# Kernel tuning notes

Measured on AMD Instinct MI355X. Metric: run time of the kernel, lower is better.

Reference implementation:

```python
import jax, jax.numpy as jnp
import numpy as np
from jax.scipy.linalg import cho_solve

BLOCKSIZE = 128   # sharded_gptc.BLOCKSIZE
PERC_DAMP = 0.01


def _get_divisible_blocksize(dim: int, blocksize_top: int) -> int:
    b = blocksize_top
    while dim % b != 0:
        b -= 1
    return b


def setup_inputs() -> dict:
    key = jax.random.key(0)
    x = jax.random.normal(key, (4, 2048, 1024), dtype=jnp.float32)
    return {"x": x, "ca": 2}


def reference(x, ca):
    # --- reshape/transpose bookkeeping from GptqHinvCollector.__call__ ---
    ca_axes = (int(ca),)
    transpose = [a for a in range(x.ndim) if a not in ca_axes] + list(ca_axes)
    x = x.transpose(transpose)
    features = int(np.prod(x.shape[-len(ca_axes):]))
    x = x.reshape((-1, features))                      # (rows, F)
    blocksize = _get_divisible_blocksize(x.shape[0], BLOCKSIZE)
    xb = x.reshape((-1, blocksize, features))          # (nblocks, bs, F)

    # --- _init_hinv_for_calibration: damped diagonal initialization ---
    diag = jnp.mean(jnp.float32(xb) ** 2, (0, 1))      # (F,)
    damp = PERC_DAMP * jnp.mean(diag)
    hinv0 = jnp.diag(jnp.ones(features, jnp.float32) / damp)  # (damp*I)^-1

    # --- compute_hinv: blocked Woodbury / Cholesky recursion over row blocks ---
    # hinv_{k+1} = (hinv_k^{-1} + B^T B)^{-1}
    #            = hinv_k - hinv_k B^T (I + B hinv_k B^T)^{-1} B hinv_k
    eye_b = jnp.eye(blocksize, dtype=jnp.float32)

    def block_update(hinv, B):
        HB = hinv @ B.T                                # (F, bs)
        S = eye_b + B @ HB                             # (bs, bs), SPD
        L = jnp.linalg.cholesky(S)
        W = cho_solve((L, True), HB.T)                 # S^{-1} (B hinv): (bs, F)
        return hinv - HB @ W, None

    hinv, _ = jax.lax.scan(block_update, hinv0, xb)

    # act_order=False -> identity permutation
    perm = jnp.arange(features, dtype=jnp.int32)

    # CALIBRATE path after init: collected_hinv = hinv, num_calibrated_batches = 1
    num_calibrated_batches = jnp.int32(1)
    return hinv * num_calibrated_batches, perm
```

## Files before the change

kernel.cpp:

```cpp
#include <hip/hip_runtime.h>
#include <math.h>

#define F 1024
#define NROWS 8192
#define NELEM (NROWS * F)

typedef unsigned short ushort_t;
typedef short bf16x8 __attribute__((ext_vector_type(8)));
typedef float f32x4 __attribute__((ext_vector_type(4)));
typedef unsigned short ushort8 __attribute__((ext_vector_type(8)));

__device__ __forceinline__ ushort_t f2bf(float f) {
  unsigned u = __float_as_uint(f);
  unsigned r = (u + 0x7fffu + ((u >> 16) & 1u)) >> 16;
  return (ushort_t)r;
}
__device__ __forceinline__ float bf2f(ushort_t b) {
  return __uint_as_float(((unsigned)b) << 16);
}

typedef const __attribute__((address_space(1))) unsigned int* gas_ptr;
typedef __attribute__((address_space(3))) unsigned int* las_ptr;
__device__ __forceinline__ void gload16(const void* g, const void* l) {
  __builtin_amdgcn_global_load_lds((gas_ptr)(unsigned long long)g,
                                   (las_ptr)(unsigned int)(unsigned long long)l,
                                   16, 0, 0);
}

__global__ __launch_bounds__(256) void tconv_kernel(const float* __restrict__ x,
                                                    ushort_t* __restrict__ xthi,
                                                    ushort_t* __restrict__ xtlo,
                                                    float* __restrict__ partial) {
    __shared__ ushort_t th[64][68];
    __shared__ ushort_t tl[64][68];
    __shared__ float sdata[256];
    int c0 = blockIdx.x * 64;
    int r0 = blockIdx.y * 64;
    int tid = threadIdx.x;
    float ss = 0.f;
#pragma unroll
    for (int i = 0; i < 4; ++i) {
        int q = tid + 256 * i;
        int r = q >> 4;
        int cq = (q & 15) << 2;
        float4 vx = *(const float4*)&x[(size_t)(r0 + r) * 1024 + c0 + cq];
        float vv[4] = {vx.x, vx.y, vx.z, vx.w};
#pragma unroll
        for (int j = 0; j < 4; ++j) {
            ss = fmaf(vv[j], vv[j], ss);
            ushort_t h = f2bf(vv[j]);
            ushort_t l = f2bf(vv[j] - bf2f(h));
            th[r][cq + j] = h;
            tl[r][cq + j] = l;
        }
    }
    sdata[tid] = ss;
    __syncthreads();
    for (int off = 128; off > 0; off >>= 1) {
        if (tid < off) sdata[tid] += sdata[tid + off];
        __syncthreads();
    }
    if (tid == 0) partial[blockIdx.y * 16 + blockIdx.x] = sdata[0];
#pragma unroll
    for (int i = 0; i < 2; ++i) {
        int q = tid + 256 * i;
        int c = q >> 3;
        int rq = (q & 7) << 3;
        ushort8 oh, ol;
#pragma unroll
        for (int j = 0; j < 8; ++j) {
            oh[j] = th[rq + j][c];
            ol[j] = tl[rq + j][c];
        }
        *(ushort8*)&xthi[(size_t)(c0 + c) * 8192 + r0 + rq] = oh;
        *(ushort8*)&xtlo[(size_t)(c0 + c) * 8192 + r0 + rq] = ol;
    }
}

__global__ void finish_damp_kernel(const float* __restrict__ partial, float* __restrict__ scal) {
    __shared__ float sdata[256];
    int tid = threadIdx.x;
    float s = 0.f;
    for (int i = tid; i < 2048; i += 256) s += partial[i];
    sdata[tid] = s;
    __syncthreads();
    for (int off = 128; off > 0; off >>= 1) {
        if (tid < off) sdata[tid] += sdata[tid + off];
        __syncthreads();
    }
    if (tid == 0) {
        float mean = sdata[0] / (float)NELEM;
        scal[1] = 0.01f * mean;
    }
}

__device__ __forceinline__ void stage128(const ushort_t* __restrict__ gp, int row0, int kk,
                                         ushort_t* sbase, int w, int lane) {
#pragma unroll
    for (int half = 0; half < 2; ++half) {
        int s = half * 256 + (w << 6) + lane;
        int r = s >> 2, pos = s & 3;
        int kc = (pos ^ ((r >> 1) & 3)) << 3;
        gload16(gp + (size_t)(row0 + r) * 8192 + kk + kc,
                sbase + (size_t)((half << 8) + (w << 6)) * 8);
    }
}

template <int NZ>
__global__ __launch_bounds__(256, 2) void syrk_mfma_kernel(
    const ushort_t* __restrict__ XThi, const ushort_t* __restrict__ XTlo,
    float* __restrict__ P)
{
    constexpr int KCH = 8192 / NZ;
    constexpr int NKT = KCH / 32;
    __shared__ ushort_t smem[2][16384];
    int id = blockIdx.x;
    int z = id & (NZ - 1), t = id / NZ;
    int bi = 0;
    while ((bi + 1) * (bi + 2) / 2 <= t) ++bi;
    int bj = t - bi * (bi + 1) / 2;
    int arow0 = bi * 128, brow0 = bj * 128;
    int k0 = z * KCH;

    int tid = threadIdx.x, lane = tid & 63, w = tid >> 6;
    int wm = w >> 1, wn = w & 1;
    int lr = lane & 15, cg = lane >> 4;

    f32x4 zero4 = {0.f, 0.f, 0.f, 0.f};
    f32x4 acc[4][4];
#pragma unroll
    for (int a = 0; a < 4; ++a)
#pragma unroll
        for (int b = 0; b < 4; ++b) acc[a][b] = zero4;

#define SYRK_STAGE(BUF, KT)                                                        \
    {                                                                              \
        ushort_t* sb = smem[BUF];                                                  \
        int kk = k0 + ((KT) << 5);                                                 \
        stage128(XThi, arow0, kk, sb + 0, w, lane);                                \
        stage128(XTlo, arow0, kk, sb + 4096, w, lane);                             \
        stage128(XThi, brow0, kk, sb + 8192, w, lane);                             \
        stage128(XTlo, brow0, kk, sb + 12288, w, lane);                            \
    }

#define SYRK_COMPUTE(BUF)                                                          \
    {                                                                              \
        const ushort_t* sb = smem[BUF];                                            \
        bf16x8 ah[4], bh[4], al[4], bl[4];                                         \
        _Pragma("unroll")                                                          \
        for (int fx = 0; fx < 4; ++fx) {                                           \
            int xo = (cg ^ ((lr >> 1) & 3)) << 3;                                  \
            int ao = ((wm << 6) + (fx << 4) + lr) * 32 + xo;                       \
            int bo = ((wn << 6) + (fx << 4) + lr) * 32 + xo;                       \
            ah[fx] = *(const bf16x8*)&sb[0 + ao];                                  \
            al[fx] = *(const bf16x8*)&sb[4096 + ao];                               \
            bh[fx] = *(const bf16x8*)&sb[8192 + bo];                               \
            bl[fx] = *(const bf16x8*)&sb[12288 + bo];                              \
        }                                                                          \
        _Pragma("unroll")                                                          \
        for (int fm = 0; fm < 4; ++fm)                                             \
            _Pragma("unroll")                                                      \
            for (int fn = 0; fn < 4; ++fn) {                                       \
                acc[fm][fn] = __builtin_amdgcn_mfma_f32_16x16x32_bf16(             \
                    ah[fm], bh[fn], acc[fm][fn], 0, 0, 0);                         \
                acc[fm][fn] = __builtin_amdgcn_mfma_f32_16x16x32_bf16(             \
                    ah[fm], bl[fn], acc[fm][fn], 0, 0, 0);                         \
                acc[fm][fn] = __builtin_amdgcn_mfma_f32_16x16x32_bf16(             \
                    al[fm], bh[fn], acc[fm][fn], 0, 0, 0);                         \
            }                                                                      \
    }

    SYRK_STAGE(0, 0)
    for (int kt = 0; kt < NKT - 1; ++kt) {
        int buf = kt & 1;
        if (buf == 0) SYRK_STAGE(1, kt + 1) else SYRK_STAGE(0, kt + 1)
        asm volatile("s_waitcnt vmcnt(8)" ::: "memory");
        __builtin_amdgcn_s_barrier();
        __builtin_amdgcn_sched_barrier(0);
        if (buf == 0) SYRK_COMPUTE(0) else SYRK_COMPUTE(1)
        __builtin_amdgcn_sched_barrier(0);
        __builtin_amdgcn_s_barrier();
    }
    asm volatile("s_waitcnt vmcnt(0)" ::: "memory");
    __builtin_amdgcn_s_barrier();
    __builtin_amdgcn_sched_barrier(0);
    if (((NKT - 1) & 1) == 0) SYRK_COMPUTE(0) else SYRK_COMPUTE(1)

    float* Pt = P + ((size_t)(t * NZ + z) << 14);
#pragma unroll
    for (int fm = 0; fm < 4; ++fm)
#pragma unroll
        for (int fn = 0; fn < 4; ++fn)
#pragma unroll
            for (int rr = 0; rr < 4; ++rr) {
                int row = (wm << 6) + fm * 16 + cg * 4 + rr;
                int col = (wn << 6) + fn * 16 + lr;
                Pt[row * 128 + col] = acc[fm][fn][rr];
            }
}

template <int NZ>
__global__ void reduceH_kernel(const float* __restrict__ P,
                               ushort_t* __restrict__ Hhi, ushort_t* __restrict__ Hlo,
                               const float* __restrict__ scal) {
    int b = blockIdx.x;
    int tile = b >> 6;
    int li = ((b & 63) << 8) + threadIdx.x;
    int bi = 0;
    while ((bi + 1) * (bi + 2) / 2 <= tile) ++bi;
    int bj = tile - bi * (bi + 1) / 2;
    const float* Pt = P + (size_t)tile * NZ * 16384;
    float s = 0.f;
#pragma unroll
    for (int z = 0; z < NZ; ++z) s += Pt[((size_t)z << 14) + li];
    int r = li >> 7, c = li & 127;
    int gi = bi * 128 + r, gj = bj * 128 + c;
    if (gi == gj) s += scal[1];
    ushort_t h = f2bf(s), l = f2bf(s - bf2f(h));
    Hhi[gi * F + gj] = h;
    Hlo[gi * F + gj] = l;
    if (bi != bj) {
        Hhi[gj * F + gi] = h;
        Hlo[gj * F + gi] = l;
    }
}

__global__ void matvec_bf16_kernel(const ushort_t* __restrict__ Hhi, const float* __restrict__ v,
                                   float* __restrict__ y, int first) {
    __shared__ float sdata[256];
    int row = blockIdx.x, tid = threadIdx.x;
    float s = 0.f;
    if (first) {
        for (int j = tid; j < F; j += 256) s += bf2f(Hhi[row * F + j]);
    } else {
        for (int j = tid; j < F; j += 256) s = fmaf(bf2f(Hhi[row * F + j]), v[j], s);
    }
    sdata[tid] = s;
    __syncthreads();
    for (int off = 128; off > 0; off >>= 1) {
        if (tid < off) sdata[tid] += sdata[tid + off];
        __syncthreads();
    }
    if (tid == 0) y[row] = sdata[0];
}

__global__ void normalize_kernel(const float* __restrict__ y, float* __restrict__ v,
                                 float* __restrict__ scal) {
    __shared__ float sdata[256];
    __shared__ float lam;
    int tid = threadIdx.x;
    float s = 0.f;
    for (int i = tid; i < F; i += 256) {
        float t = y[i];
        s = fmaf(t, t, s);
    }
    sdata[tid] = s;
    __syncthreads();
    for (int off = 128; off > 0; off >>= 1) {
        if (tid < off) sdata[tid] += sdata[tid + off];
        __syncthreads();
    }
    if (tid == 0) {
        lam = sqrtf(sdata[0]);
        scal[2] = lam;
        scal[3] = 1.0f / (1.05f * lam);
    }
    __syncthreads();
    float il = 1.0f / lam;
    for (int i = tid; i < F; i += 256) v[i] = y[i] * il;
}

__global__ void initX1_kernel(const ushort_t* __restrict__ Hhi, const ushort_t* __restrict__ Hlo,
                              ushort_t* __restrict__ Xhi, ushort_t* __restrict__ Xlo,
                              const float* __restrict__ scal) {
    int idx0 = (blockIdx.x * 256 + threadIdx.x) * 4;
    float c = scal[3];
    float c2 = c * c;
#pragma unroll
    for (int k = 0; k < 4; ++k) {
        int idx = idx0 + k;
        float hv = bf2f(Hhi[idx]) + bf2f(Hlo[idx]);
        float val = -c2 * hv + (((idx >> 10) == (idx & 1023)) ? 2.f * c : 0.f);
        ushort_t h = f2bf(val);
        Xhi[idx] = h;
        Xlo[idx] = f2bf(val - bf2f(h));
    }
}

__device__ __forceinline__ void stage64(const ushort_t* __restrict__ gp, int row0, int kk,
                                        ushort_t* sbase, int tid) {
    int r = tid >> 2, pos = tid & 3;
    int kc = (pos ^ ((r >> 1) & 3)) << 3;
    gload16(gp + (size_t)(row0 + r) * 1024 + kk + kc, sbase + (size_t)(tid >> 6 << 9));
}

template <int TERMS, int MODE>
__global__ __launch_bounds__(256) void ns_gemm_kernel(
    const ushort_t* __restrict__ Ahi, const ushort_t* __restrict__ Alo,
    const ushort_t* __restrict__ Bhi, const ushort_t* __restrict__ Blo,
    const ushort_t* __restrict__ Xchi, const ushort_t* __restrict__ Xclo,
    ushort_t* __restrict__ Ohi, ushort_t* __restrict__ Olo,
    float* __restrict__ Of)
{
    constexpr int SLOT = (TERMS == 3) ? 8192 : 4096;
    __shared__ ushort_t smem[4 * SLOT];
    int tid = threadIdx.x, lane = tid & 63, w = tid >> 6;
    int wm = w >> 1, wn = w & 1;
    int row0 = blockIdx.y * 64, col0 = blockIdx.x * 64;
    int lr = lane & 15, cg = lane >> 4;

    f32x4 zero4 = {0.f, 0.f, 0.f, 0.f};
    f32x4 acc[2][2];
#pragma unroll
    for (int a = 0; a < 2; ++a)
#pragma unroll
        for (int b = 0; b < 2; ++b) acc[a][b] = zero4;

#define NS_STAGE(KT)                                                               \
    {                                                                              \
        ushort_t* sb = smem + (size_t)((KT) & 3) * SLOT;                           \
        int kk = (KT) << 5;                                                        \
        stage64(Ahi, row0, kk, sb + 0, tid);                                       \
        stage64(Bhi, col0, kk, sb + 2048, tid);                                    \
        if constexpr (TERMS == 3) {                                                \
            stage64(Alo, row0, kk, sb + 4096, tid);                                \
            stage64(Blo, col0, kk, sb + 6144, tid);                                \
        }                                                                          \
    }

#define NS_COMPUTE(KT)                                                             \
    {                                                                              \
        const ushort_t* sb = smem + (size_t)((KT) & 3) * SLOT;                     \
        bf16x8 ah[2], bh[2], al[2], bl[2];                                         \
        _Pragma("unroll")                                                          \
        for (int fx = 0; fx < 2; ++fx) {                                           \
            int xo = (cg ^ ((lr >> 1) & 3)) << 3;                                  \
            int ao = ((wm << 5) + (fx << 4) + lr) * 32 + xo;                       \
            int bo = ((wn << 5) + (fx << 4) + lr) * 32 + xo;                       \
            ah[fx] = *(const bf16x8*)&sb[0 + ao];                                  \
            bh[fx] = *(const bf16x8*)&sb[2048 + bo];                               \
            if constexpr (TERMS == 3) {                                            \
                al[fx] = *(const bf16x8*)&sb[4096 + ao];                           \
                bl[fx] = *(const bf16x8*)&sb[6144 + bo];                           \
            }                                                                      \
        }                                                                          \
        _Pragma("unroll")                                                          \
        for (int fm = 0; fm < 2; ++fm)                                             \
            _Pragma("unroll")                                                      \
            for (int fn = 0; fn < 2; ++fn) {                                       \
                acc[fm][fn] = __builtin_amdgcn_mfma_f32_16x16x32_bf16(             \
                    ah[fm], bh[fn], acc[fm][fn], 0, 0, 0);                         \
                if constexpr (TERMS == 3) {                                        \
                    acc[fm][fn] = __builtin_amdgcn_mfma_f32_16x16x32_bf16(         \
                        ah[fm], bl[fn], acc[fm][fn], 0, 0, 0);                     \
                    acc[fm][fn] = __builtin_amdgcn_mfma_f32_16x16x32_bf16(         \
                        al[fm], bh[fn], acc[fm][fn], 0, 0, 0);                     \
                }                                                                  \
            }                                                                      \
    }

    NS_STAGE(0)
    NS_STAGE(1)
    for (int kt = 0; kt < 30; ++kt) {
        NS_STAGE(kt + 2)
        if constexpr (TERMS == 3) { asm volatile("s_waitcnt vmcnt(8)" ::: "memory"); }
        else                      { asm volatile("s_waitcnt vmcnt(4)" ::: "memory"); }
        __builtin_amdgcn_s_barrier();
        __builtin_amdgcn_sched_barrier(0);
        NS_COMPUTE(kt)
        __builtin_amdgcn_sched_barrier(0);
    }
    if constexpr (TERMS == 3) { asm volatile("s_waitcnt vmcnt(4)" ::: "memory"); }
    else                      { asm volatile("s_waitcnt vmcnt(2)" ::: "memory"); }
    __builtin_amdgcn_s_barrier();
    __builtin_amdgcn_sched_barrier(0);
    NS_COMPUTE(30)
    asm volatile("s_waitcnt vmcnt(0)" ::: "memory");
    __builtin_amdgcn_s_barrier();
    __builtin_amdgcn_sched_barrier(0);
    NS_COMPUTE(31)

#pragma unroll
    for (int fm = 0; fm < 2; ++fm)
#pragma unroll
        for (int fn = 0; fn < 2; ++fn)
#pragma unroll
            for (int rr = 0; rr < 4; ++rr) {
                int r = row0 + (wm << 5) + fm * 16 + cg * 4 + rr;
                int c = col0 + (wn << 5) + fn * 16 + lr;
                size_t idx = (size_t)r * F + c;
                float val = acc[fm][fn][rr];
                if constexpr (MODE == 0) {
                    ushort_t h = f2bf(val);
                    Ohi[idx] = h;
                    Olo[idx] = f2bf(val - bf2f(h));
                } else {
                    float xc = bf2f(Xchi[idx]) + bf2f(Xclo[idx]);
                    val = 2.0f * xc - val;
                    if constexpr (MODE == 1) {
                        ushort_t h = f2bf(val);
                        Ohi[idx] = h;
                        Olo[idx] = f2bf(val - bf2f(h));
                    } else {
                        Of[idx] = val;
                    }
                }
            }
    if constexpr (MODE == 2) {
        if (blockIdx.x == 0 && blockIdx.y == 0) {
            int i0 = tid * 4;
#pragma unroll
            for (int k = 0; k < 4; ++k)
                Of[(size_t)F * F + i0 + k] = (float)(i0 + k);
        }
    }
}

__global__ void sumsq_partial_kernel(const float* __restrict__ x, float* __restrict__ partial) {
    __shared__ float sdata[256];
    int tid = threadIdx.x;
    int base = blockIdx.x * 4096;
    float s = 0.f;
    for (int i = tid; i < 4096; i += 256) {
        float v = x[base + i];
        s = fmaf(v, v, s);
    }
    sdata[tid] = s;
    __syncthreads();
    for (int off = 128; off > 0; off >>= 1) {
        if (tid < off) sdata[tid] += sdata[tid + off];
        __syncthreads();
    }
    if (tid == 0) partial[blockIdx.x] = sdata[0];
}

__global__ void init_v_kernel(float* __restrict__ v) {
    int i = blockIdx.x * 256 + threadIdx.x;
    if (i < F) v[i] = 1.0f;
}

__global__ void matvec_kernel(const float* __restrict__ H, const float* __restrict__ v,
                              float* __restrict__ y) {
    __shared__ float sdata[256];
    int row = blockIdx.x, tid = threadIdx.x;
    float s = 0.f;
    for (int j = tid; j < F; j += 256) s = fmaf(H[row * F + j], v[j], s);
    sdata[tid] = s;
    __syncthreads();
    for (int off = 128; off > 0; off >>= 1) {
        if (tid < off) sdata[tid] += sdata[tid + off];
        __syncthreads();
    }
    if (tid == 0) y[row] = sdata[0];
}

__global__ __launch_bounds__(256) void syrk_kernel(const float* __restrict__ X,
                                                   float* __restrict__ H,
                                                   const float* __restrict__ scal) {
    __shared__ float LA[16][64];
    __shared__ float LB[16][64];
    int tx = threadIdx.x, ty = threadIdx.y;
    int t = ty * 16 + tx;
    int i0 = blockIdx.y * 64, j0 = blockIdx.x * 64;
    int lk = t >> 4;
    int lc = (t & 15) << 2;
    float acc[4][4] = {};
    for (int k0 = 0; k0 < NROWS; k0 += 16) {
        int r = (k0 + lk) * F;
        float4 a4 = *(const float4*)&X[r + i0 + lc];
        float4 b4 = *(const float4*)&X[r + j0 + lc];
        __syncthreads();
        *(float4*)&LA[lk][lc] = a4;
        *(float4*)&LB[lk][lc] = b4;
        __syncthreads();
#pragma unroll
        for (int kk = 0; kk < 16; ++kk) {
            float4 a = *(const float4*)&LA[kk][ty << 2];
            float4 b = *(const float4*)&LB[kk][tx << 2];
            float av[4] = {a.x, a.y, a.z, a.w};
            float bv[4] = {b.x, b.y, b.z, b.w};
#pragma unroll
            for (int rr = 0; rr < 4; ++rr)
#pragma unroll
                for (int cc = 0; cc < 4; ++cc)
                    acc[rr][cc] = fmaf(av[rr], bv[cc], acc[rr][cc]);
        }
    }
    float damp = scal[1];
#pragma unroll
    for (int rr = 0; rr < 4; ++rr) {
        int i = i0 + (ty << 2) + rr;
#pragma unroll
        for (int cc = 0; cc < 4; ++cc) {
            int j = j0 + (tx << 2) + cc;
            float v = acc[rr][cc];
            if (i == j) v += damp;
            H[i * F + j] = v;
        }
    }
}

__global__ void init_X_kernel(float* __restrict__ A, const float* __restrict__ scal) {
    int idx = blockIdx.x * 256 + threadIdx.x;
    int i = idx >> 10, j = idx & (F - 1);
    A[idx] = (i == j) ? scal[3] : 0.0f;
}

__global__ __launch_bounds__(256) void gemm_nn_kernel(const float* __restrict__ A,
                                                      const float* __restrict__ Bm,
                                                      float* __restrict__ C,
                                                      const float* __restrict__ D,
                                                      int mode) {
    __shared__ float LA[16][64];
    __shared__ float LB[16][64];
    int tx = threadIdx.x, ty = threadIdx.y;
    int t = ty * 16 + tx;
    int i0 = blockIdx.y * 64, j0 = blockIdx.x * 64;
    int aii = t >> 2;
    int akq = (t & 3) << 2;
    int bkk = t >> 4;
    int bjq = (t & 15) << 2;
    float acc[4][4] = {};
    for (int k0 = 0; k0 < F; k0 += 16) {
        float4 a4 = *(const float4*)&A[(i0 + aii) * F + k0 + akq];
        float4 b4 = *(const float4*)&Bm[(k0 + bkk) * F + j0 + bjq];
        __syncthreads();
        LA[akq + 0][aii] = a4.x;
        LA[akq + 1][aii] = a4.y;
        LA[akq + 2][aii] = a4.z;
        LA[akq + 3][aii] = a4.w;
        *(float4*)&LB[bkk][bjq] = b4;
        __syncthreads();
#pragma unroll
        for (int kk = 0; kk < 16; ++kk) {
            float4 a = *(const float4*)&LA[kk][ty << 2];
            float4 b = *(const float4*)&LB[kk][tx << 2];
            float av[4] = {a.x, a.y, a.z, a.w};
            float bv[4] = {b.x, b.y, b.z, b.w};
#pragma unroll
            for (int rr = 0; rr < 4; ++rr)
#pragma unroll
                for (int cc = 0; cc < 4; ++cc)
                    acc[rr][cc] = fmaf(av[rr], bv[cc], acc[rr][cc]);
        }
    }
#pragma unroll
    for (int rr = 0; rr < 4; ++rr) {
        int i = i0 + (ty << 2) + rr;
#pragma unroll
        for (int cc = 0; cc < 4; ++cc) {
            int j = j0 + (tx << 2) + cc;
            float v = acc[rr][cc];
            if (mode == 1) v = 2.0f * D[i * F + j] - v;
            C[i * F + j] = v;
        }
    }
}

__global__ void finalize_kernel(const float* __restrict__ A, float* __restrict__ out) {
    int idx = blockIdx.x * 256 + threadIdx.x;
    if (idx < F * F) out[idx] = A[idx];
    else if (idx < F * F + F) out[idx] = (float)(idx - F * F);
}

extern "C" void kernel_launch(void* const* d_in, const int* in_sizes, int n_in,
                              void* d_out, int out_size, void* d_ws, size_t ws_size,
                              hipStream_t stream) {
    const float* x = (const float*)d_in[0];
    float* out = (float*)d_out;

    char* base = (char*)d_ws;
    size_t off = 0;
    auto alloc = [&](size_t bytes) -> char* {
        char* p = base + off;
        off += bytes;
        off = (off + 255) & ~(size_t)255;
        return p;
    };
    float*    scal = (float*)alloc(64 * 4);
    float*    part = (float*)alloc(2048 * 4);
    ushort_t* XThi = (ushort_t*)alloc((size_t)NELEM * 2);
    ushort_t* XTlo = (ushort_t*)alloc((size_t)NELEM * 2);
    ushort_t* Hhi  = (ushort_t*)alloc((size_t)F * F * 2);
    ushort_t* Hlo  = (ushort_t*)alloc((size_t)F * F * 2);
    ushort_t* X0hi = (ushort_t*)alloc((size_t)F * F * 2);
    ushort_t* X0lo = (ushort_t*)alloc((size_t)F * F * 2);
    ushort_t* X1hi = (ushort_t*)alloc((size_t)F * F * 2);
    ushort_t* X1lo = (ushort_t*)alloc((size_t)F * F * 2);
    ushort_t* Shi  = (ushort_t*)alloc((size_t)F * F * 2);
    ushort_t* Slo  = (ushort_t*)alloc((size_t)F * F * 2);
    float*    v    = (float*)alloc(F * 4);
    float*    y    = (float*)alloc(F * 4);
    float*    P    = (float*)alloc(0);
    size_t base_off = off;
    size_t need8  = base_off + (size_t)36 * 8  * 16384 * 4;
    size_t need16 = base_off + (size_t)36 * 16 * 16384 * 4;

    if (ws_size >= need8) {
        tconv_kernel<<<dim3(16, 128), 256, 0, stream>>>(x, XThi, XTlo, part);
        finish_damp_kernel<<<1, 256, 0, stream>>>(part, scal);

        if (ws_size >= need16) {
            syrk_mfma_kernel<16><<<36 * 16, 256, 0, stream>>>(XThi, XTlo, P);
            reduceH_kernel<16><<<36 * 64, 256, 0, stream>>>(P, Hhi, Hlo, scal);
        } else {
            syrk_mfma_kernel<8><<<36 * 8, 256, 0, stream>>>(XThi, XTlo, P);
            reduceH_kernel<8><<<36 * 64, 256, 0, stream>>>(P, Hhi, Hlo, scal);
        }

        matvec_bf16_kernel<<<F, 256, 0, stream>>>(Hhi, v, y, 1);
        normalize_kernel<<<1, 256, 0, stream>>>(y, v, scal);
        matvec_bf16_kernel<<<F, 256, 0, stream>>>(Hhi, v, y, 0);
        normalize_kernel<<<1, 256, 0, stream>>>(y, v, scal);

        initX1_kernel<<<1024, 256, 0, stream>>>(Hhi, Hlo, X0hi, X0lo, scal);

        ushort_t* xch = X0hi; ushort_t* xcl = X0lo;
        ushort_t* xnh = X1hi; ushort_t* xnl = X1lo;
        dim3 g(16, 16);
        for (int it = 0; it < 4; ++it) {
            bool last = (it == 3);
            if (it < 1) {
                ns_gemm_kernel<1, 0><<<g, 256, 0, stream>>>(xch, xcl, Hhi, Hlo,
                                                            nullptr, nullptr, Shi, Slo, nullptr);
                ns_gemm_kernel<1, 1><<<g, 256, 0, stream>>>(Shi, Slo, xch, xcl,
                                                            xch, xcl, xnh, xnl, nullptr);
            } else {
                ns_gemm_kernel<3, 0><<<g, 256, 0, stream>>>(xch, xcl, Hhi, Hlo,
                                                            nullptr, nullptr, Shi, Slo, nullptr);
                if (last)
                    ns_gemm_kernel<3, 2><<<g, 256, 0, stream>>>(Shi, Slo, xch, xcl,
                                                                xch, xcl, nullptr, nullptr, out);
                else
                    ns_gemm_kernel<3, 1><<<g, 256, 0, stream>>>(Shi, Slo, xch, xcl,
                                                                xch, xcl, xnh, xnl, nullptr);
            }
            ushort_t* th = xch; xch = xnh; xnh = th;
            ushort_t* tl = xcl; xcl = xnl; xnl = tl;
        }
    } else {
        float* ws = (float*)d_ws;
        float* fscal    = ws;
        float* fpartial = ws + 64;
        float* fH  = ws + 4096;
        float* fA  = fH + F * F;
        float* fB  = fA + F * F;
        float* fv  = fB + F * F;
        float* fy  = fv + F;
        float* R = out;

        sumsq_partial_kernel<<<2048, 256, 0, stream>>>(x, fpartial);
        finish_damp_kernel<<<1, 256, 0, stream>>>(fpartial, fscal);

        dim3 grid16(16, 16), blk16(16, 16);
        syrk_kernel<<<grid16, blk16, 0, stream>>>(x, fH, fscal);

        init_v_kernel<<<4, 256, 0, stream>>>(fv);
        for (int it = 0; it < 12; ++it) {
            matvec_kernel<<<F, 256, 0, stream>>>(fH, fv, fy);
            normalize_kernel<<<1, 256, 0, stream>>>(fy, fv, fscal);
        }

        init_X_kernel<<<(F * F) / 256, 256, 0, stream>>>(fA, fscal);
        float* Xc = fA;
        float* Xn = fB;
        for (int it = 0; it < 8; ++it) {
            gemm_nn_kernel<<<grid16, blk16, 0, stream>>>(fH, Xc, R, nullptr, 0);
            gemm_nn_kernel<<<grid16, blk16, 0, stream>>>(Xc, R, Xn, Xc, 1);
            float* tmp = Xc; Xc = Xn; Xn = tmp;
        }

        finalize_kernel<<<(F * F + F + 255) / 256, 256, 0, stream>>>(Xc, out);
    }
}
```

Measured before the change: 171.6 us.

## Fuse damp and normalize kernels, drop a power iteration, specialize diagonal SYRK tiles

Folds the damping reduction into reduceH and the eigenvalue normalization into initX1, which removes several single-block launches. The power iteration goes from two matvecs to one, using a crude bound (norm/32 with a 1.15 safety factor) for the largest eigenvalue. SYRK is fixed to an 8-way K split, and diagonal tiles now stage only the A operand and reuse it as B. Together these cut launch count and memory traffic, but the looser eigenvalue estimate can slow Newton-Schulz convergence with the fixed iteration count, and every reduceH block now redundantly repeats the 2048-element damp reduction.

```diff
diff --git a/kernel.cpp b/kernel.cpp
--- a/kernel.cpp
+++ b/kernel.cpp
@@ -77,23 +77,6 @@
     }
 }
 
-__global__ void finish_damp_kernel(const float* __restrict__ partial, float* __restrict__ scal) {
-    __shared__ float sdata[256];
-    int tid = threadIdx.x;
-    float s = 0.f;
-    for (int i = tid; i < 2048; i += 256) s += partial[i];
-    sdata[tid] = s;
-    __syncthreads();
-    for (int off = 128; off > 0; off >>= 1) {
-        if (tid < off) sdata[tid] += sdata[tid + off];
-        __syncthreads();
-    }
-    if (tid == 0) {
-        float mean = sdata[0] / (float)NELEM;
-        scal[1] = 0.01f * mean;
-    }
-}
-
 __device__ __forceinline__ void stage128(const ushort_t* __restrict__ gp, int row0, int kk,
                                          ushort_t* sbase, int w, int lane) {
 #pragma unroll
@@ -106,21 +89,18 @@
     }
 }
 
-template <int NZ>
 __global__ __launch_bounds__(256, 2) void syrk_mfma_kernel(
     const ushort_t* __restrict__ XThi, const ushort_t* __restrict__ XTlo,
     float* __restrict__ P)
 {
-    constexpr int KCH = 8192 / NZ;
-    constexpr int NKT = KCH / 32;
     __shared__ ushort_t smem[2][16384];
     int id = blockIdx.x;
-    int z = id & (NZ - 1), t = id / NZ;
+    int z = id & 7, t = id >> 3;
     int bi = 0;
     while ((bi + 1) * (bi + 2) / 2 <= t) ++bi;
     int bj = t - bi * (bi + 1) / 2;
     int arow0 = bi * 128, brow0 = bj * 128;
-    int k0 = z * KCH;
+    int k0 = z * 1024;
 
     int tid = threadIdx.x, lane = tid & 63, w = tid >> 6;
     int wm = w >> 1, wn = w & 1;
@@ -133,7 +113,7 @@
 #pragma unroll
         for (int b = 0; b < 4; ++b) acc[a][b] = zero4;
 
-#define SYRK_STAGE(BUF, KT)                                                        \
+#define SY_STAGE_F(BUF, KT)                                                        \
     {                                                                              \
         ushort_t* sb = smem[BUF];                                                  \
         int kk = k0 + ((KT) << 5);                                                 \
@@ -143,7 +123,15 @@
         stage128(XTlo, brow0, kk, sb + 12288, w, lane);                            \
     }
 
-#define SYRK_COMPUTE(BUF)                                                          \
+#define SY_STAGE_D(BUF, KT)                                                        \
+    {                                                                              \
+        ushort_t* sb = smem[BUF];                                                  \
+        int kk = k0 + ((KT) << 5);                                                 \
+        stage128(XThi, arow0, kk, sb + 0, w, lane);                                \
+        stage128(XTlo, arow0, kk, sb + 4096, w, lane);                             \
+    }
+
+#define SY_COMP(BUF, BH, BL)                                                       \
     {                                                                              \
         const ushort_t* sb = smem[BUF];                                            \
         bf16x8 ah[4], bh[4], al[4], bl[4];                                         \
@@ -154,8 +142,8 @@
             int bo = ((wn << 6) + (fx << 4) + lr) * 32 + xo;                       \
             ah[fx] = *(const bf16x8*)&sb[0 + ao];                                  \
             al[fx] = *(const bf16x8*)&sb[4096 + ao];                               \
-            bh[fx] = *(const bf16x8*)&sb[8192 + bo];                               \
-            bl[fx] = *(const bf16x8*)&sb[12288 + bo];                              \
+            bh[fx] = *(const bf16x8*)&sb[(BH) + bo];                               \
+            bl[fx] = *(const bf16x8*)&sb[(BL) + bo];                               \
         }                                                                          \
         _Pragma("unroll")                                                          \
         for (int fm = 0; fm < 4; ++fm)                                             \
@@ -170,23 +158,41 @@
             }                                                                      \
     }
 
-    SYRK_STAGE(0, 0)
-    for (int kt = 0; kt < NKT - 1; ++kt) {
-        int buf = kt & 1;
-        if (buf == 0) SYRK_STAGE(1, kt + 1) else SYRK_STAGE(0, kt + 1)
-        asm volatile("s_waitcnt vmcnt(8)" ::: "memory");
+    if (bi != bj) {
+        SY_STAGE_F(0, 0)
+        for (int kt = 0; kt < 31; ++kt) {
+            int buf = kt & 1;
+            if (buf == 0) SY_STAGE_F(1, kt + 1) else SY_STAGE_F(0, kt + 1)
+            asm volatile("s_waitcnt vmcnt(8)" ::: "memory");
+            __builtin_amdgcn_s_barrier();
+            __builtin_amdgcn_sched_barrier(0);
+            if (buf == 0) SY_COMP(0, 8192, 12288) else SY_COMP(1, 8192, 12288)
+            __builtin_amdgcn_sched_barrier(0);
+            __builtin_amdgcn_s_barrier();
+        }
+        asm volatile("s_waitcnt vmcnt(0)" ::: "memory");
         __builtin_amdgcn_s_barrier();
         __builtin_amdgcn_sched_barrier(0);
-        if (buf == 0) SYRK_COMPUTE(0) else SYRK_COMPUTE(1)
+        SY_COMP(1, 8192, 12288)
+    } else {
+        SY_STAGE_D(0, 0)
+        for (int kt = 0; kt < 31; ++kt) {
+            int buf = kt & 1;
+            if (buf == 0) SY_STAGE_D(1, kt + 1) else SY_STAGE_D(0, kt + 1)
+            asm volatile("s_waitcnt vmcnt(4)" ::: "memory");
+            __builtin_amdgcn_s_barrier();
+            __builtin_amdgcn_sched_barrier(0);
+            if (buf == 0) SY_COMP(0, 0, 4096) else SY_COMP(1, 0, 4096)
+            __builtin_amdgcn_sched_barrier(0);
+            __builtin_amdgcn_s_barrier();
+        }
+        asm volatile("s_waitcnt vmcnt(0)" ::: "memory");
+        __builtin_amdgcn_s_barrier();
         __builtin_amdgcn_sched_barrier(0);
-        __builtin_amdgcn_s_barrier();
-    }
-    asm volatile("s_waitcnt vmcnt(0)" ::: "memory");
-    __builtin_amdgcn_s_barrier();
-    __builtin_amdgcn_sched_barrier(0);
-    if (((NKT - 1) & 1) == 0) SYRK_COMPUTE(0) else SYRK_COMPUTE(1)
-
-    float* Pt = P + ((size_t)(t * NZ + z) << 14);
+        SY_COMP(1, 0, 4096)
+    }
+
+    float* Pt = P + ((size_t)(t * 8 + z) << 14);
 #pragma unroll
     for (int fm = 0; fm < 4; ++fm)
 #pragma unroll
@@ -199,23 +205,33 @@
             }
 }
 
-template <int NZ>
-__global__ void reduceH_kernel(const float* __restrict__ P,
-                               ushort_t* __restrict__ Hhi, ushort_t* __restrict__ Hlo,
-                               const float* __restrict__ scal) {
+__global__ void reduceH_kernel(const float* __restrict__ P, const float* __restrict__ part,
+                               ushort_t* __restrict__ Hhi, ushort_t* __restrict__ Hlo) {
+    __shared__ float red[256];
+    int tid = threadIdx.x;
+    float s0 = 0.f;
+    for (int i = tid; i < 2048; i += 256) s0 += part[i];
+    red[tid] = s0;
+    __syncthreads();
+    for (int off = 128; off > 0; off >>= 1) {
+        if (tid < off) red[tid] += red[tid + off];
+        __syncthreads();
+    }
+    float damp = 0.01f * (red[0] / (float)NELEM);
+
     int b = blockIdx.x;
     int tile = b >> 6;
-    int li = ((b & 63) << 8) + threadIdx.x;
+    int li = ((b & 63) << 8) + tid;
     int bi = 0;
     while ((bi + 1) * (bi + 2) / 2 <= tile) ++bi;
     int bj = tile - bi * (bi + 1) / 2;
-    const float* Pt = P + (size_t)tile * NZ * 16384;
+    const float* Pt = P + ((size_t)tile << 17);
     float s = 0.f;
 #pragma unroll
-    for (int z = 0; z < NZ; ++z) s += Pt[((size_t)z << 14) + li];
+    for (int z = 0; z < 8; ++z) s += Pt[((size_t)z << 14) + li];
     int r = li >> 7, c = li & 127;
     int gi = bi * 128 + r, gj = bj * 128 + c;
-    if (gi == gj) s += scal[1];
+    if (gi == gj) s += damp;
     ushort_t h = f2bf(s), l = f2bf(s - bf2f(h));
     Hhi[gi * F + gj] = h;
     Hlo[gi * F + gj] = l;
@@ -244,38 +260,24 @@
     if (tid == 0) y[row] = sdata[0];
 }
 
-__global__ void normalize_kernel(const float* __restrict__ y, float* __restrict__ v,
-                                 float* __restrict__ scal) {
-    __shared__ float sdata[256];
-    __shared__ float lam;
-    int tid = threadIdx.x;
-    float s = 0.f;
-    for (int i = tid; i < F; i += 256) {
-        float t = y[i];
-        s = fmaf(t, t, s);
-    }
-    sdata[tid] = s;
-    __syncthreads();
-    for (int off = 128; off > 0; off >>= 1) {
-        if (tid < off) sdata[tid] += sdata[tid + off];
-        __syncthreads();
-    }
-    if (tid == 0) {
-        lam = sqrtf(sdata[0]);
-        scal[2] = lam;
-        scal[3] = 1.0f / (1.05f * lam);
-    }
-    __syncthreads();
-    float il = 1.0f / lam;
-    for (int i = tid; i < F; i += 256) v[i] = y[i] * il;
-}
-
 __global__ void initX1_kernel(const ushort_t* __restrict__ Hhi, const ushort_t* __restrict__ Hlo,
                               ushort_t* __restrict__ Xhi, ushort_t* __restrict__ Xlo,
-                              const float* __restrict__ scal) {
-    int idx0 = (blockIdx.x * 256 + threadIdx.x) * 4;
-    float c = scal[3];
+                              const float* __restrict__ y, float* __restrict__ scal) {
+    __shared__ float red[256];
+    int tid = threadIdx.x;
+    float4 a = ((const float4*)y)[tid];
+    float s = a.x * a.x + a.y * a.y + a.z * a.z + a.w * a.w;
+    red[tid] = s;
+    __syncthreads();
+    for (int off = 128; off > 0; off >>= 1) {
+        if (tid < off) red[tid] += red[tid + off];
+        __syncthreads();
+    }
+    float lam = sqrtf(red[0]) * (1.0f / 32.0f);
+    float c = 1.0f / (1.15f * lam);
+    if (blockIdx.x == 0 && tid == 0) { scal[2] = lam; scal[3] = c; }
     float c2 = c * c;
+    int idx0 = (blockIdx.x * 256 + tid) * 4;
 #pragma unroll
     for (int k = 0; k < 4; ++k) {
         int idx = idx0 + k;
@@ -434,6 +436,23 @@
     if (tid == 0) partial[blockIdx.x] = sdata[0];
 }
 
+__global__ void finish_damp_kernel(const float* __restrict__ partial, float* __restrict__ scal) {
+    __shared__ float sdata[256];
+    int tid = threadIdx.x;
+    float s = 0.f;
+    for (int i = tid; i < 2048; i += 256) s += partial[i];
+    sdata[tid] = s;
+    __syncthreads();
+    for (int off = 128; off > 0; off >>= 1) {
+        if (tid < off) sdata[tid] += sdata[tid + off];
+        __syncthreads();
+    }
+    if (tid == 0) {
+        float mean = sdata[0] / (float)NELEM;
+        scal[1] = 0.01f * mean;
+    }
+}
+
 __global__ void init_v_kernel(float* __restrict__ v) {
     int i = blockIdx.x * 256 + threadIdx.x;
     if (i < F) v[i] = 1.0f;
@@ -452,6 +471,32 @@
         __syncthreads();
     }
     if (tid == 0) y[row] = sdata[0];
+}
+
+__global__ void normalize_kernel(const float* __restrict__ y, float* __restrict__ v,
+                                 float* __restrict__ scal) {
+    __shared__ float sdata[256];
+    __shared__ float lam;
+    int tid = threadIdx.x;
+    float s = 0.f;
+    for (int i = tid; i < F; i += 256) {
+        float t = y[i];
+        s = fmaf(t, t, s);
+    }
+    sdata[tid] = s;
+    __syncthreads();
+    for (int off = 128; off > 0; off >>= 1) {
+        if (tid < off) sdata[tid] += sdata[tid + off];
+        __syncthreads();
+    }
+    if (tid == 0) {
+        lam = sqrtf(sdata[0]);
+        scal[2] = lam;
+        scal[3] = 1.0f / (1.05f * lam);
+    }
+    __syncthreads();
+    float il = 1.0f / lam;
+    for (int i = tid; i < F; i += 256) v[i] = y[i] * il;
 }
 
 __global__ __launch_bounds__(256) void syrk_kernel(const float* __restrict__ X,
@@ -591,29 +636,18 @@
     ushort_t* Slo  = (ushort_t*)alloc((size_t)F * F * 2);
     float*    v    = (float*)alloc(F * 4);
     float*    y    = (float*)alloc(F * 4);
-    float*    P    = (float*)alloc(0);
-    size_t base_off = off;
-    size_t need8  = base_off + (size_t)36 * 8  * 16384 * 4;
-    size_t need16 = base_off + (size_t)36 * 16 * 16384 * 4;
-
-    if (ws_size >= need8) {
+    float*    P    = (float*)alloc((size_t)36 * 8 * 16384 * 4);
+    size_t need = off;
+
+    if (ws_size >= need) {
         tconv_kernel<<<dim3(16, 128), 256, 0, stream>>>(x, XThi, XTlo, part);
-        finish_damp_kernel<<<1, 256, 0, stream>>>(part, scal);
-
-        if (ws_size >= need16) {
-            syrk_mfma_kernel<16><<<36 * 16, 256, 0, stream>>>(XThi, XTlo, P);
-            reduceH_kernel<16><<<36 * 64, 256, 0, stream>>>(P, Hhi, Hlo, scal);
-        } else {
-            syrk_mfma_kernel<8><<<36 * 8, 256, 0, stream>>>(XThi, XTlo, P);
-            reduceH_kernel<8><<<36 * 64, 256, 0, stream>>>(P, Hhi, Hlo, scal);
-        }
+
+        syrk_mfma_kernel<<<288, 256, 0, stream>>>(XThi, XTlo, P);
+        reduceH_kernel<<<36 * 64, 256, 0, stream>>>(P, part, Hhi, Hlo);
 
         matvec_bf16_kernel<<<F, 256, 0, stream>>>(Hhi, v, y, 1);
-        normalize_kernel<<<1, 256, 0, stream>>>(y, v, scal);
-        matvec_bf16_kernel<<<F, 256, 0, stream>>>(Hhi, v, y, 0);
-        normalize_kernel<<<1, 256, 0, stream>>>(y, v, scal);
-
-        initX1_kernel<<<1024, 256, 0, stream>>>(Hhi, Hlo, X0hi, X0lo, scal);
+
+        initX1_kernel<<<1024, 256, 0, stream>>>(Hhi, Hlo, X0hi, X0lo, y, scal);
 
         ushort_t* xch = X0hi; ushort_t* xcl = X0lo;
         ushort_t* xnh = X1hi; ushort_t* xnl = X1lo;
```

Result: faster. 163.4 us (-4.7%).
